# Performance work log

Measured on AMD Instinct MI355X. Metric: run time of the kernel, lower is better.

## Reference

```python
import jax, jax.numpy as jnp
import numpy as np

B, T, C, H = 4, 2048, 1024, 16
D = C // H


def setup_inputs() -> dict:
    key = jax.random.key(0)
    ks = jax.random.split(key, 5)
    s = C ** -0.5  # keep linear outputs O(1) like standard init
    x = jax.random.normal(ks[0], (B, T, C), dtype=jnp.float32)
    Wq = jax.random.normal(ks[1], (C, C), dtype=jnp.float32) * s
    Wk = jax.random.normal(ks[2], (C, C), dtype=jnp.float32) * s
    Wv = jax.random.normal(ks[3], (C, C), dtype=jnp.float32) * s
    Wproj = jax.random.normal(ks[4], (C, C), dtype=jnp.float32) * s
    alpha_raw = jnp.zeros((1, H, 1, 1), dtype=jnp.float32)
    beta_raw = jnp.zeros((1, H, 1, 1), dtype=jnp.float32)
    state = jnp.zeros((B, H, D, D), dtype=jnp.float32)
    return dict(x=x, Wq=Wq, Wk=Wk, Wv=Wv, Wproj=Wproj,
                alpha_raw=alpha_raw, beta_raw=beta_raw, state=state)


def reference(x, Wq, Wk, Wv, Wproj, alpha_raw, beta_raw, state):
    Bx, Tx, Cx = x.shape
    Hn = alpha_raw.shape[1]
    Dh = Cx // Hn
    # projections (torch Linear: x @ W^T), split heads -> (B, H, T, D)
    def proj(W):
        return (x @ W.T).reshape(Bx, Tx, Hn, Dh).transpose(0, 2, 1, 3)
    q, k, v = proj(Wq), proj(Wk), proj(Wv)
    # F.normalize(k, dim=-1) with eps=1e-12
    k = k / jnp.maximum(jnp.linalg.norm(k, axis=-1, keepdims=True), 1e-12)
    alpha = jax.nn.sigmoid(alpha_raw) * 0.5  # (1, H, 1, 1)
    beta = jax.nn.sigmoid(beta_raw) * 0.5

    def step(st, qkv):
        qt, kt, vt = qkv  # each (B, H, D)
        # y_t = q_t @ state^T
        y = jnp.einsum('bhe,bhde->bhd', qt, st)
        # Mk = state @ k_t
        Mk = jnp.einsum('bhde,bhe->bhd', st, kt)
        st = st - alpha * jnp.einsum('bhd,bhe->bhde', Mk, kt) \
                + beta * jnp.einsum('bhd,bhe->bhde', vt, kt)
        return st, y

    # scan over time: (T, B, H, D)
    qT = q.transpose(2, 0, 1, 3)
    kT = k.transpose(2, 0, 1, 3)
    vT = v.transpose(2, 0, 1, 3)
    state_f, ys = jax.lax.scan(step, state, (qT, kT, vT))
    y = ys.transpose(1, 0, 2, 3).reshape(Bx, Tx, Cx)  # (B, T, C)
    out = y @ Wproj.T
    return out, state_f
```

## Files before the change

kernel.cpp:

```cpp
#include <hip/hip_runtime.h>
#include <hip/hip_bf16.h>
#include <cstdint>

#define B_ 4
#define T_ 2048
#define C_ 1024
#define H_ 16
#define D_ 64
#define NC_ 32
#define L_ 64

typedef __attribute__((ext_vector_type(8))) short bf16x8;
typedef __attribute__((ext_vector_type(4))) float f32x4;

static __device__ __forceinline__ unsigned short f2bf(float f) {
  unsigned u = __float_as_uint(f);
  u += 0x7fff + ((u >> 16) & 1);
  return (unsigned short)(u >> 16);
}
static __device__ __forceinline__ float bf2f(unsigned short b) {
  return __uint_as_float(((unsigned)b) << 16);
}
static __device__ __forceinline__ int swz128(int row, int byte) {
  return row * 128 + (byte ^ ((row & 7) << 4));
}

__global__ __launch_bounds__(256) void cvt_kernel(const float* __restrict__ src,
                                                  unsigned short* __restrict__ dst, int n) {
  int i = (blockIdx.x * 256 + threadIdx.x) * 4;
  if (i >= n) return;
  float4 v = *reinterpret_cast<const float4*>(src + i);
  ushort4 o;
  o.x = f2bf(v.x); o.y = f2bf(v.y); o.z = f2bf(v.z); o.w = f2bf(v.w);
  *reinterpret_cast<ushort4*>(dst + i) = o;
}

template<int OUT_BF16>
__global__ __launch_bounds__(256) void gemm_bt(const unsigned short* __restrict__ A,
                                               const unsigned short* __restrict__ Bw,
                                               void* __restrict__ Cp,
                                               int M, int N, int K) {
  __shared__ __align__(16) unsigned short sA[128 * 32];
  __shared__ __align__(16) unsigned short sB[128 * 32];
  const int tid = threadIdx.x;
  const int wid = tid >> 6, lane = tid & 63;
  const int wm = wid >> 1, wn = wid & 1;
  const long blockM = (long)blockIdx.y * 128;
  const long blockN = (long)blockIdx.x * 128;

  f32x4 acc[4][4] = {};

  const int ar = lane >> 2;
  const int ac = (lane & 3) * 8;
  const unsigned short* Abase = A + (blockM + wid * 32 + ar) * (long)K + ac;
  const unsigned short* Bbase = Bw + (blockN + wid * 32 + ar) * (long)K + ac;
  char* sAb = (char*)sA + wid * 2048;
  char* sBb = (char*)sB + wid * 2048;

  for (int k0 = 0; k0 < K; k0 += 32) {
    __syncthreads();
    __builtin_amdgcn_global_load_lds((const __attribute__((address_space(1))) void*)(Abase + k0),
                                     (__attribute__((address_space(3))) void*)(sAb), 16, 0, 0);
    __builtin_amdgcn_global_load_lds((const __attribute__((address_space(1))) void*)(Abase + 16 * (long)K + k0),
                                     (__attribute__((address_space(3))) void*)(sAb + 1024), 16, 0, 0);
    __builtin_amdgcn_global_load_lds((const __attribute__((address_space(1))) void*)(Bbase + k0),
                                     (__attribute__((address_space(3))) void*)(sBb), 16, 0, 0);
    __builtin_amdgcn_global_load_lds((const __attribute__((address_space(1))) void*)(Bbase + 16 * (long)K + k0),
                                     (__attribute__((address_space(3))) void*)(sBb + 1024), 16, 0, 0);
    __syncthreads();

    const int koff = (lane >> 4) * 8;
    const int rA = wm * 64 + (lane & 15);
    const int rB = wn * 64 + (lane & 15);
    bf16x8 af[4], bfr[4];
#pragma unroll
    for (int m = 0; m < 4; ++m)
      af[m] = *reinterpret_cast<const bf16x8*>(&sA[(rA + m * 16) * 32 + koff]);
#pragma unroll
    for (int n = 0; n < 4; ++n)
      bfr[n] = *reinterpret_cast<const bf16x8*>(&sB[(rB + n * 16) * 32 + koff]);
#pragma unroll
    for (int m = 0; m < 4; ++m)
#pragma unroll
      for (int n = 0; n < 4; ++n)
        acc[m][n] = __builtin_amdgcn_mfma_f32_16x16x32_bf16(af[m], bfr[n], acc[m][n], 0, 0, 0);
  }

  const int cr = (lane >> 4) * 4;
  const int cc = lane & 15;
#pragma unroll
  for (int m = 0; m < 4; ++m) {
    long R = blockM + wm * 64 + m * 16 + cr;
#pragma unroll
    for (int n = 0; n < 4; ++n) {
      long Cc = blockN + wn * 64 + n * 16 + cc;
#pragma unroll
      for (int r = 0; r < 4; ++r) {
        if (OUT_BF16)
          ((unsigned short*)Cp)[(R + r) * (long)N + Cc] = f2bf(acc[m][n][r]);
        else
          ((float*)Cp)[(R + r) * (long)N + Cc] = acc[m][n][r];
      }
    }
  }
}

__global__ __launch_bounds__(256) void chunk_prep(
    unsigned short* __restrict__ qkv,
    const float* __restrict__ a_raw, const float* __restrict__ b_raw,
    unsigned short* __restrict__ Ubuf, unsigned short* __restrict__ Wbuf,
    unsigned short* __restrict__ SLbuf) {
  __shared__ __align__(16) unsigned short sK[64 * 64];
  __shared__ __align__(16) unsigned short sQ[64 * 64];
  __shared__ __align__(16) unsigned short sV[64 * 64];
  __shared__ float sA[64 * 64];

  const int blk = blockIdx.x;
  const int bh = blk >> 5, c = blk & 31;
  const int b = bh >> 4, h = bh & 15;
  const int tid = threadIdx.x;
  const int wid = tid >> 6, lane = tid & 63;

  const float alpha = 0.5f / (1.f + __expf(-a_raw[h]));
  const float beta  = 0.5f / (1.f + __expf(-b_raw[h]));

  {
    const int row = tid >> 2, cg = tid & 3;
    unsigned short* gp = qkv + (long)(b * 2048 + c * 64 + row) * 3072 + h * 64 + cg * 16;
    bf16x8 q0 = *(const bf16x8*)(gp);
    bf16x8 q1 = *(const bf16x8*)(gp + 8);
    bf16x8 k0 = *(const bf16x8*)(gp + 1024);
    bf16x8 k1 = *(const bf16x8*)(gp + 1024 + 8);
    bf16x8 v0 = *(const bf16x8*)(gp + 2048);
    bf16x8 v1 = *(const bf16x8*)(gp + 2048 + 8);
    float kf[16];
    float ss = 0.f;
#pragma unroll
    for (int i = 0; i < 8; ++i) { kf[i] = bf2f((unsigned short)k0[i]); ss += kf[i] * kf[i]; }
#pragma unroll
    for (int i = 0; i < 8; ++i) { kf[8 + i] = bf2f((unsigned short)k1[i]); ss += kf[8 + i] * kf[8 + i]; }
    ss += __shfl_xor(ss, 1);
    ss += __shfl_xor(ss, 2);
    const float inv = 1.f / fmaxf(sqrtf(ss), 1e-12f);
    bf16x8 n0, n1;
#pragma unroll
    for (int i = 0; i < 8; ++i) { n0[i] = (short)f2bf(kf[i] * inv); n1[i] = (short)f2bf(kf[8 + i] * inv); }
    *(bf16x8*)((char*)sK + swz128(row, cg * 32)) = n0;
    *(bf16x8*)((char*)sK + swz128(row, cg * 32 + 16)) = n1;
    *(bf16x8*)(gp + 1024) = n0;
    *(bf16x8*)(gp + 1024 + 8) = n1;
    *(bf16x8*)((char*)sQ + swz128(row, cg * 32)) = q0;
    *(bf16x8*)((char*)sQ + swz128(row, cg * 32 + 16)) = q1;
    *(bf16x8*)((char*)sV + row * 128 + cg * 32) = v0;
    *(bf16x8*)((char*)sV + row * 128 + cg * 32 + 16) = v1;
  }
  __syncthreads();

  const int rfrag = lane & 15, koff = (lane >> 4) * 8, crow = (lane >> 4) * 4;
  const int w2 = wid & 1;
  if (wid < 2) {
#pragma unroll
    for (int mt = 0; mt < 2; ++mt) {
      const int m = w2 * 2 + mt;
      const int ra = 16 * m + rfrag;
      f32x4 acc[4] = {};
#pragma unroll
      for (int ks = 0; ks < 2; ++ks) {
        bf16x8 af = *(const bf16x8*)((const char*)sK + swz128(ra, ks * 64 + koff * 2));
#pragma unroll
        for (int n = 0; n < 4; ++n) {
          bf16x8 bf = *(const bf16x8*)((const char*)sK + swz128(16 * n + rfrag, ks * 64 + koff * 2));
          acc[n] = __builtin_amdgcn_mfma_f32_16x16x32_bf16(af, bf, acc[n], 0, 0, 0);
        }
      }
#pragma unroll
      for (int n = 0; n < 4; ++n)
#pragma unroll
        for (int r = 0; r < 4; ++r)
          sA[(16 * m + crow + r) * 64 + 16 * n + rfrag] = acc[n][r];
    }
  } else {
#pragma unroll
    for (int mt = 0; mt < 2; ++mt) {
      const int m = w2 * 2 + mt;
      const int ra = 16 * m + rfrag;
      f32x4 acc[4] = {};
#pragma unroll
      for (int ks = 0; ks < 2; ++ks) {
        bf16x8 af = *(const bf16x8*)((const char*)sQ + swz128(ra, ks * 64 + koff * 2));
#pragma unroll
        for (int n = 0; n < 4; ++n) {
          bf16x8 bf = *(const bf16x8*)((const char*)sK + swz128(16 * n + rfrag, ks * 64 + koff * 2));
          acc[n] = __builtin_amdgcn_mfma_f32_16x16x32_bf16(af, bf, acc[n], 0, 0, 0);
        }
      }
#pragma unroll
      for (int n = 0; n < 4; ++n)
#pragma unroll
        for (int r = 0; r < 4; ++r) {
          int t = 16 * m + crow + r, j = 16 * n + rfrag;
          SLbuf[(long)blk * 4096 + t * 64 + j] = (j < t) ? f2bf(acc[n][r]) : (unsigned short)0;
        }
    }
  }
  __syncthreads();

  if (wid < 2) {
    const int d = lane;
    float x[64];
#pragma unroll
    for (int t = 0; t < 64; ++t) {
      float rhs;
      if (wid == 0) rhs = beta * bf2f(sV[t * 64 + d]);
      else          rhs = alpha * bf2f(*(const unsigned short*)((const char*)sK + swz128(t, 2 * d)));
      float s = 0.f;
#pragma unroll
      for (int j = 0; j < t; ++j) s = fmaf(sA[t * 64 + j], x[j], s);
      x[t] = rhs - alpha * s;
    }
    unsigned short* ob = (wid == 0 ? Ubuf : Wbuf) + (long)blk * 4096 + d;
#pragma unroll
    for (int t = 0; t < 64; ++t) ob[t * 64] = f2bf(x[t]);
  }
}

__global__ __launch_bounds__(256) void chunk_scan(
    const unsigned short* __restrict__ qkv,
    const unsigned short* __restrict__ Ubuf, const unsigned short* __restrict__ Wbuf,
    const unsigned short* __restrict__ SLbuf,
    const float* __restrict__ state_in, unsigned short* __restrict__ ybuf,
    float* __restrict__ state_out) {
  __shared__ __align__(16) unsigned short sQ[64 * 64];
  __shared__ __align__(16) unsigned short sW[64 * 64];
  __shared__ __align__(16) unsigned short sSL[64 * 64];
  __shared__ __align__(16) unsigned short sKT[64 * 64];
  __shared__ __align__(16) unsigned short sU[64 * 32];
  __shared__ __align__(16) unsigned short sGT[32 * 64];
  __shared__ __align__(16) unsigned short sS[32 * 64];

  const int blk = blockIdx.x;
  const int bh = blk >> 1, dh = blk & 1;
  const int b = bh >> 4, h = bh & 15;
  const int tid = threadIdx.x, wid = tid >> 6, lane = tid & 63;
  const int rfrag = lane & 15, koff = (lane >> 4) * 8, crow = (lane >> 4) * 4;
  const int row = tid >> 2, cg = tid & 3;

  const unsigned short* gpb = qkv + (long)(b * 2048 + row) * 3072 + h * 64 + cg * 16;
  const long tbb = ((long)(bh * 32) * 64 + row) * 64 + cg * 16;
  const long ubb = ((long)(bh * 32) * 64 + row) * 64 + dh * 32 + cg * 8;

  bf16x8 qv0, qv1, kv0, kv1, wv0, wv1, sl0, sl1, uv;
  {
    const unsigned short* gp = gpb;
    qv0 = *(const bf16x8*)gp;
    qv1 = *(const bf16x8*)(gp + 8);
    kv0 = *(const bf16x8*)(gp + 1024);
    kv1 = *(const bf16x8*)(gp + 1024 + 8);
    wv0 = *(const bf16x8*)(Wbuf + tbb);
    wv1 = *(const bf16x8*)(Wbuf + tbb + 8);
    sl0 = *(const bf16x8*)(SLbuf + tbb);
    sl1 = *(const bf16x8*)(SLbuf + tbb + 8);
    uv  = *(const bf16x8*)(Ubuf + ubb);
  }

  const int mS = wid & 1, nS0 = (wid >> 1) * 2;
  f32x4 sacc[2];
#pragma unroll
  for (int nn = 0; nn < 2; ++nn)
#pragma unroll
    for (int r = 0; r < 4; ++r)
      sacc[nn][r] = state_in[(long)bh * 4096 + (dh * 32 + 16 * mS + crow + r) * 64 + 16 * (nS0 + nn) + rfrag];
#pragma unroll
  for (int nn = 0; nn < 2; ++nn)
#pragma unroll
    for (int r = 0; r < 4; ++r) {
      int dr = 16 * mS + crow + r, e = 16 * (nS0 + nn) + rfrag;
      *(unsigned short*)((char*)sS + swz128(dr, 2 * e)) = f2bf(sacc[nn][r]);
    }

  for (int c = 0; c < NC_; ++c) {
    *(bf16x8*)((char*)sQ + swz128(row, cg * 32)) = qv0;
    *(bf16x8*)((char*)sQ + swz128(row, cg * 32 + 16)) = qv1;
    *(bf16x8*)((char*)sW + swz128(row, cg * 32)) = wv0;
    *(bf16x8*)((char*)sW + swz128(row, cg * 32 + 16)) = wv1;
    *(bf16x8*)((char*)sSL + swz128(row, cg * 32)) = sl0;
    *(bf16x8*)((char*)sSL + swz128(row, cg * 32 + 16)) = sl1;
#pragma unroll
    for (int i = 0; i < 8; ++i) {
      *(unsigned short*)((char*)sKT + swz128(cg * 16 + i, 2 * row)) = (unsigned short)kv0[i];
      *(unsigned short*)((char*)sKT + swz128(cg * 16 + 8 + i, 2 * row)) = (unsigned short)kv1[i];
    }
    *(bf16x8*)((char*)sU + (row * 32 + cg * 8) * 2) = uv;

    {
      const int cn = (c + 1 < NC_) ? c + 1 : c;
      const unsigned short* gp = gpb + (long)cn * 64 * 3072;
      const long tb = tbb + (long)cn * 4096;
      qv0 = *(const bf16x8*)gp;
      qv1 = *(const bf16x8*)(gp + 8);
      kv0 = *(const bf16x8*)(gp + 1024);
      kv1 = *(const bf16x8*)(gp + 1024 + 8);
      wv0 = *(const bf16x8*)(Wbuf + tb);
      wv1 = *(const bf16x8*)(Wbuf + tb + 8);
      sl0 = *(const bf16x8*)(SLbuf + tb);
      sl1 = *(const bf16x8*)(SLbuf + tb + 8);
      uv  = *(const bf16x8*)(Ubuf + ubb + (long)cn * 4096);
    }
    __syncthreads();

    const int ta = 16 * wid + rfrag;
    f32x4 p[2] = {};
    f32x4 yac[2] = {};
#pragma unroll
    for (int ks = 0; ks < 2; ++ks) {
      bf16x8 afw = *(const bf16x8*)((const char*)sW + swz128(ta, ks * 64 + koff * 2));
      bf16x8 afq = *(const bf16x8*)((const char*)sQ + swz128(ta, ks * 64 + koff * 2));
#pragma unroll
      for (int n = 0; n < 2; ++n) {
        bf16x8 bf = *(const bf16x8*)((const char*)sS + swz128(16 * n + rfrag, ks * 64 + koff * 2));
        p[n] = __builtin_amdgcn_mfma_f32_16x16x32_bf16(afw, bf, p[n], 0, 0, 0);
        yac[n] = __builtin_amdgcn_mfma_f32_16x16x32_bf16(afq, bf, yac[n], 0, 0, 0);
      }
    }
#pragma unroll
    for (int n = 0; n < 2; ++n)
#pragma unroll
      for (int r = 0; r < 4; ++r) {
        int t = 16 * wid + crow + r, dl = 16 * n + rfrag;
        float g = bf2f(sU[t * 32 + dl]) - p[n][r];
        *(unsigned short*)((char*)sGT + swz128(dl, 2 * t)) = f2bf(g);
      }
    __syncthreads();

#pragma unroll
    for (int ks = 0; ks < 2; ++ks) {
      bf16x8 af = *(const bf16x8*)((const char*)sSL + swz128(ta, ks * 64 + koff * 2));
#pragma unroll
      for (int n = 0; n < 2; ++n) {
        bf16x8 bf = *(const bf16x8*)((const char*)sGT + swz128(16 * n + rfrag, ks * 64 + koff * 2));
        yac[n] = __builtin_amdgcn_mfma_f32_16x16x32_bf16(af, bf, yac[n], 0, 0, 0);
      }
    }
#pragma unroll
    for (int n = 0; n < 2; ++n)
#pragma unroll
      for (int r = 0; r < 4; ++r) {
        int t = 16 * wid + crow + r;
        ybuf[(long)(b * 2048 + c * 64 + t) * 1024 + h * 64 + dh * 32 + 16 * n + rfrag] = f2bf(yac[n][r]);
      }
#pragma unroll
    for (int ks = 0; ks < 2; ++ks) {
      bf16x8 af = *(const bf16x8*)((const char*)sGT + swz128(16 * mS + rfrag, ks * 64 + koff * 2));
#pragma unroll
      for (int nn = 0; nn < 2; ++nn) {
        bf16x8 bf = *(const bf16x8*)((const char*)sKT + swz128(16 * (nS0 + nn) + rfrag, ks * 64 + koff * 2));
        sacc[nn] = __builtin_amdgcn_mfma_f32_16x16x32_bf16(af, bf, sacc[nn], 0, 0, 0);
      }
    }
    __syncthreads();
#pragma unroll
    for (int nn = 0; nn < 2; ++nn)
#pragma unroll
      for (int r = 0; r < 4; ++r) {
        int dr = 16 * mS + crow + r, e = 16 * (nS0 + nn) + rfrag;
        *(unsigned short*)((char*)sS + swz128(dr, 2 * e)) = f2bf(sacc[nn][r]);
      }
  }

#pragma unroll
  for (int nn = 0; nn < 2; ++nn)
#pragma unroll
    for (int r = 0; r < 4; ++r)
      state_out[(long)bh * 4096 + (dh * 32 + 16 * mS + crow + r) * 64 + 16 * (nS0 + nn) + rfrag] = sacc[nn][r];
}

extern "C" void kernel_launch(void* const* d_in, const int* in_sizes, int n_in,
                              void* d_out, int out_size, void* d_ws, size_t ws_size,
                              hipStream_t stream) {
  (void)in_sizes; (void)n_in; (void)out_size; (void)ws_size;
  const float* x     = (const float*)d_in[0];
  const float* Wq    = (const float*)d_in[1];
  const float* Wk    = (const float*)d_in[2];
  const float* Wv    = (const float*)d_in[3];
  const float* Wproj = (const float*)d_in[4];
  const float* a_raw = (const float*)d_in[5];
  const float* b_raw = (const float*)d_in[6];
  const float* state = (const float*)d_in[7];

  char* ws = (char*)d_ws;
  unsigned short* xbf = (unsigned short*)ws;
  unsigned short* W3  = (unsigned short*)(ws + (16l << 20));
  unsigned short* Wp  = (unsigned short*)(ws + (22l << 20));
  unsigned short* qkv = (unsigned short*)(ws + (24l << 20));
  unsigned short* Ub  = (unsigned short*)(ws + (72l << 20));
  unsigned short* Wb  = (unsigned short*)(ws + (88l << 20));
  unsigned short* SLb = (unsigned short*)(ws + (104l << 20));
  float* out = (float*)d_out;
  float* state_out = out + (long)B_ * T_ * C_;

  cvt_kernel<<<dim3(8192), dim3(256), 0, stream>>>(x, xbf, 8388608);
  cvt_kernel<<<dim3(1024), dim3(256), 0, stream>>>(Wq, W3, 1048576);
  cvt_kernel<<<dim3(1024), dim3(256), 0, stream>>>(Wk, W3 + 1048576, 1048576);
  cvt_kernel<<<dim3(1024), dim3(256), 0, stream>>>(Wv, W3 + 2097152, 1048576);
  cvt_kernel<<<dim3(1024), dim3(256), 0, stream>>>(Wproj, Wp, 1048576);

  gemm_bt<1><<<dim3(3072 / 128, 8192 / 128), dim3(256), 0, stream>>>(xbf, W3, (void*)qkv, 8192, 3072, 1024);

  chunk_prep<<<dim3(2048), dim3(256), 0, stream>>>(qkv, a_raw, b_raw, Ub, Wb, SLb);
  chunk_scan<<<dim3(128), dim3(256), 0, stream>>>(qkv, Ub, Wb, SLb, state, xbf, state_out);

  gemm_bt<0><<<dim3(1024 / 128, 8192 / 128), dim3(256), 0, stream>>>(xbf, Wp, (void*)out, 8192, 1024, 1024);
}
```

Measured before the change: 216.2 us.

## Split chunk scan state rows four ways and merge weight conversions

The sequential chunk_scan kernel now splits each head's 64-row state into four 16-row slices instead of two 32-row halves. This doubles the grid from 128 to 256 blocks, so more of the GPU's compute units take part in the serial scan and each block does less MFMA work per chunk. The cost is redundant work: every block still loads and stages the full Q, K, W and SL tiles, so global and LDS traffic per head roughly doubles. Separately, the four weight-conversion launches are merged into one kernel to cut launch overhead.

```diff
diff --git a/kernel.cpp b/kernel.cpp
--- a/kernel.cpp
+++ b/kernel.cpp
@@ -29,6 +29,22 @@
                                                   unsigned short* __restrict__ dst, int n) {
   int i = (blockIdx.x * 256 + threadIdx.x) * 4;
   if (i >= n) return;
+  float4 v = *reinterpret_cast<const float4*>(src + i);
+  ushort4 o;
+  o.x = f2bf(v.x); o.y = f2bf(v.y); o.z = f2bf(v.z); o.w = f2bf(v.w);
+  *reinterpret_cast<ushort4*>(dst + i) = o;
+}
+
+__global__ __launch_bounds__(256) void cvt_w_kernel(const float* __restrict__ wq,
+                                                    const float* __restrict__ wk,
+                                                    const float* __restrict__ wv,
+                                                    const float* __restrict__ wp,
+                                                    unsigned short* __restrict__ W3,
+                                                    unsigned short* __restrict__ Wp) {
+  const int g = blockIdx.x >> 10;
+  const float* src = (g == 0) ? wq : (g == 1) ? wk : (g == 2) ? wv : wp;
+  unsigned short* dst = (g < 3) ? (W3 + (long)g * 1048576) : Wp;
+  int i = ((blockIdx.x & 1023) * 256 + threadIdx.x) * 4;
   float4 v = *reinterpret_cast<const float4*>(src + i);
   ushort4 o;
   o.x = f2bf(v.x); o.y = f2bf(v.y); o.z = f2bf(v.z); o.w = f2bf(v.w);
@@ -234,12 +250,12 @@
   __shared__ __align__(16) unsigned short sW[64 * 64];
   __shared__ __align__(16) unsigned short sSL[64 * 64];
   __shared__ __align__(16) unsigned short sKT[64 * 64];
-  __shared__ __align__(16) unsigned short sU[64 * 32];
-  __shared__ __align__(16) unsigned short sGT[32 * 64];
-  __shared__ __align__(16) unsigned short sS[32 * 64];
+  __shared__ __align__(16) unsigned short sU[64 * 16];
+  __shared__ __align__(16) unsigned short sGT[16 * 64];
+  __shared__ __align__(16) unsigned short sS[16 * 64];
 
   const int blk = blockIdx.x;
-  const int bh = blk >> 1, dh = blk & 1;
+  const int bh = blk >> 2, dq = blk & 3;
   const int b = bh >> 4, h = bh & 15;
   const int tid = threadIdx.x, wid = tid >> 6, lane = tid & 63;
   const int rfrag = lane & 15, koff = (lane >> 4) * 8, crow = (lane >> 4) * 4;
@@ -247,36 +263,28 @@
 
   const unsigned short* gpb = qkv + (long)(b * 2048 + row) * 3072 + h * 64 + cg * 16;
   const long tbb = ((long)(bh * 32) * 64 + row) * 64 + cg * 16;
-  const long ubb = ((long)(bh * 32) * 64 + row) * 64 + dh * 32 + cg * 8;
+  const long ubb = ((long)(bh * 32) * 64 + (tid >> 1)) * 64 + dq * 16 + (tid & 1) * 8;
 
   bf16x8 qv0, qv1, kv0, kv1, wv0, wv1, sl0, sl1, uv;
   {
-    const unsigned short* gp = gpb;
-    qv0 = *(const bf16x8*)gp;
-    qv1 = *(const bf16x8*)(gp + 8);
-    kv0 = *(const bf16x8*)(gp + 1024);
-    kv1 = *(const bf16x8*)(gp + 1024 + 8);
+    qv0 = *(const bf16x8*)gpb;
+    qv1 = *(const bf16x8*)(gpb + 8);
+    kv0 = *(const bf16x8*)(gpb + 1024);
+    kv1 = *(const bf16x8*)(gpb + 1024 + 8);
     wv0 = *(const bf16x8*)(Wbuf + tbb);
     wv1 = *(const bf16x8*)(Wbuf + tbb + 8);
     sl0 = *(const bf16x8*)(SLbuf + tbb);
     sl1 = *(const bf16x8*)(SLbuf + tbb + 8);
-    uv  = *(const bf16x8*)(Ubuf + ubb);
-  }
-
-  const int mS = wid & 1, nS0 = (wid >> 1) * 2;
-  f32x4 sacc[2];
-#pragma unroll
-  for (int nn = 0; nn < 2; ++nn)
-#pragma unroll
-    for (int r = 0; r < 4; ++r)
-      sacc[nn][r] = state_in[(long)bh * 4096 + (dh * 32 + 16 * mS + crow + r) * 64 + 16 * (nS0 + nn) + rfrag];
-#pragma unroll
-  for (int nn = 0; nn < 2; ++nn)
-#pragma unroll
-    for (int r = 0; r < 4; ++r) {
-      int dr = 16 * mS + crow + r, e = 16 * (nS0 + nn) + rfrag;
-      *(unsigned short*)((char*)sS + swz128(dr, 2 * e)) = f2bf(sacc[nn][r]);
-    }
+    uv = (tid < 128) ? *(const bf16x8*)(Ubuf + ubb) : bf16x8{};
+  }
+
+  f32x4 sacc;
+#pragma unroll
+  for (int r = 0; r < 4; ++r)
+    sacc[r] = state_in[(long)bh * 4096 + (dq * 16 + crow + r) * 64 + 16 * wid + rfrag];
+#pragma unroll
+  for (int r = 0; r < 4; ++r)
+    *(unsigned short*)((char*)sS + swz128(crow + r, 2 * (16 * wid + rfrag))) = f2bf(sacc[r]);
 
   for (int c = 0; c < NC_; ++c) {
     *(bf16x8*)((char*)sQ + swz128(row, cg * 32)) = qv0;
@@ -290,7 +298,7 @@
       *(unsigned short*)((char*)sKT + swz128(cg * 16 + i, 2 * row)) = (unsigned short)kv0[i];
       *(unsigned short*)((char*)sKT + swz128(cg * 16 + 8 + i, 2 * row)) = (unsigned short)kv1[i];
     }
-    *(bf16x8*)((char*)sU + (row * 32 + cg * 8) * 2) = uv;
+    if (tid < 128) *(bf16x8*)((char*)sU + ((tid >> 1) * 16 + (tid & 1) * 8) * 2) = uv;
 
     {
       const int cn = (c + 1 < NC_) ? c + 1 : c;
@@ -304,74 +312,55 @@
       wv1 = *(const bf16x8*)(Wbuf + tb + 8);
       sl0 = *(const bf16x8*)(SLbuf + tb);
       sl1 = *(const bf16x8*)(SLbuf + tb + 8);
-      uv  = *(const bf16x8*)(Ubuf + ubb + (long)cn * 4096);
+      if (tid < 128) uv = *(const bf16x8*)(Ubuf + ubb + (long)cn * 4096);
     }
     __syncthreads();
 
     const int ta = 16 * wid + rfrag;
-    f32x4 p[2] = {};
-    f32x4 yac[2] = {};
+    f32x4 p = {};
+    f32x4 yac = {};
 #pragma unroll
     for (int ks = 0; ks < 2; ++ks) {
       bf16x8 afw = *(const bf16x8*)((const char*)sW + swz128(ta, ks * 64 + koff * 2));
       bf16x8 afq = *(const bf16x8*)((const char*)sQ + swz128(ta, ks * 64 + koff * 2));
-#pragma unroll
-      for (int n = 0; n < 2; ++n) {
-        bf16x8 bf = *(const bf16x8*)((const char*)sS + swz128(16 * n + rfrag, ks * 64 + koff * 2));
-        p[n] = __builtin_amdgcn_mfma_f32_16x16x32_bf16(afw, bf, p[n], 0, 0, 0);
-        yac[n] = __builtin_amdgcn_mfma_f32_16x16x32_bf16(afq, bf, yac[n], 0, 0, 0);
-      }
-    }
-#pragma unroll
-    for (int n = 0; n < 2; ++n)
-#pragma unroll
-      for (int r = 0; r < 4; ++r) {
-        int t = 16 * wid + crow + r, dl = 16 * n + rfrag;
-        float g = bf2f(sU[t * 32 + dl]) - p[n][r];
-        *(unsigned short*)((char*)sGT + swz128(dl, 2 * t)) = f2bf(g);
-      }
+      bf16x8 bS = *(const bf16x8*)((const char*)sS + swz128(rfrag, ks * 64 + koff * 2));
+      p = __builtin_amdgcn_mfma_f32_16x16x32_bf16(afw, bS, p, 0, 0, 0);
+      yac = __builtin_amdgcn_mfma_f32_16x16x32_bf16(afq, bS, yac, 0, 0, 0);
+    }
+#pragma unroll
+    for (int r = 0; r < 4; ++r) {
+      int t = 16 * wid + crow + r;
+      float g = bf2f(sU[t * 16 + rfrag]) - p[r];
+      *(unsigned short*)((char*)sGT + swz128(rfrag, 2 * t)) = f2bf(g);
+    }
     __syncthreads();
 
 #pragma unroll
     for (int ks = 0; ks < 2; ++ks) {
-      bf16x8 af = *(const bf16x8*)((const char*)sSL + swz128(ta, ks * 64 + koff * 2));
-#pragma unroll
-      for (int n = 0; n < 2; ++n) {
-        bf16x8 bf = *(const bf16x8*)((const char*)sGT + swz128(16 * n + rfrag, ks * 64 + koff * 2));
-        yac[n] = __builtin_amdgcn_mfma_f32_16x16x32_bf16(af, bf, yac[n], 0, 0, 0);
-      }
-    }
-#pragma unroll
-    for (int n = 0; n < 2; ++n)
-#pragma unroll
-      for (int r = 0; r < 4; ++r) {
-        int t = 16 * wid + crow + r;
-        ybuf[(long)(b * 2048 + c * 64 + t) * 1024 + h * 64 + dh * 32 + 16 * n + rfrag] = f2bf(yac[n][r]);
-      }
+      bf16x8 aSL = *(const bf16x8*)((const char*)sSL + swz128(ta, ks * 64 + koff * 2));
+      bf16x8 bGT = *(const bf16x8*)((const char*)sGT + swz128(rfrag, ks * 64 + koff * 2));
+      yac = __builtin_amdgcn_mfma_f32_16x16x32_bf16(aSL, bGT, yac, 0, 0, 0);
+    }
+#pragma unroll
+    for (int r = 0; r < 4; ++r) {
+      int t = 16 * wid + crow + r;
+      ybuf[(long)(b * 2048 + c * 64 + t) * 1024 + h * 64 + dq * 16 + rfrag] = f2bf(yac[r]);
+    }
 #pragma unroll
     for (int ks = 0; ks < 2; ++ks) {
-      bf16x8 af = *(const bf16x8*)((const char*)sGT + swz128(16 * mS + rfrag, ks * 64 + koff * 2));
-#pragma unroll
-      for (int nn = 0; nn < 2; ++nn) {
-        bf16x8 bf = *(const bf16x8*)((const char*)sKT + swz128(16 * (nS0 + nn) + rfrag, ks * 64 + koff * 2));
-        sacc[nn] = __builtin_amdgcn_mfma_f32_16x16x32_bf16(af, bf, sacc[nn], 0, 0, 0);
-      }
-    }
-    __syncthreads();
-#pragma unroll
-    for (int nn = 0; nn < 2; ++nn)
-#pragma unroll
-      for (int r = 0; r < 4; ++r) {
-        int dr = 16 * mS + crow + r, e = 16 * (nS0 + nn) + rfrag;
-        *(unsigned short*)((char*)sS + swz128(dr, 2 * e)) = f2bf(sacc[nn][r]);
-      }
-  }
-
-#pragma unroll
-  for (int nn = 0; nn < 2; ++nn)
+      bf16x8 aGT = *(const bf16x8*)((const char*)sGT + swz128(rfrag, ks * 64 + koff * 2));
+      bf16x8 bKT = *(const bf16x8*)((const char*)sKT + swz128(16 * wid + rfrag, ks * 64 + koff * 2));
+      sacc = __builtin_amdgcn_mfma_f32_16x16x32_bf16(aGT, bKT, sacc, 0, 0, 0);
+    }
+    __syncthreads();
 #pragma unroll
     for (int r = 0; r < 4; ++r)
-      state_out[(long)bh * 4096 + (dh * 32 + 16 * mS + crow + r) * 64 + 16 * (nS0 + nn) + rfrag] = sacc[nn][r];
+      *(unsigned short*)((char*)sS + swz128(crow + r, 2 * (16 * wid + rfrag))) = f2bf(sacc[r]);
+  }
+
+#pragma unroll
+  for (int r = 0; r < 4; ++r)
+    state_out[(long)bh * 4096 + (dq * 16 + crow + r) * 64 + 16 * wid + rfrag] = sacc[r];
 }
 
 extern "C" void kernel_launch(void* const* d_in, const int* in_sizes, int n_in,
@@ -399,15 +388,12 @@
   float* state_out = out + (long)B_ * T_ * C_;
 
   cvt_kernel<<<dim3(8192), dim3(256), 0, stream>>>(x, xbf, 8388608);
-  cvt_kernel<<<dim3(1024), dim3(256), 0, stream>>>(Wq, W3, 1048576);
-  cvt_kernel<<<dim3(1024), dim3(256), 0, stream>>>(Wk, W3 + 1048576, 1048576);
-  cvt_kernel<<<dim3(1024), dim3(256), 0, stream>>>(Wv, W3 + 2097152, 1048576);
-  cvt_kernel<<<dim3(1024), dim3(256), 0, stream>>>(Wproj, Wp, 1048576);
+  cvt_w_kernel<<<dim3(4096), dim3(256), 0, stream>>>(Wq, Wk, Wv, Wproj, W3, Wp);
 
   gemm_bt<1><<<dim3(3072 / 128, 8192 / 128), dim3(256), 0, stream>>>(xbf, W3, (void*)qkv, 8192, 3072, 1024);
 
   chunk_prep<<<dim3(2048), dim3(256), 0, stream>>>(qkv, a_raw, b_raw, Ub, Wb, SLb);
-  chunk_scan<<<dim3(128), dim3(256), 0, stream>>>(qkv, Ub, Wb, SLb, state, xbf, state_out);
+  chunk_scan<<<dim3(256), dim3(256), 0, stream>>>(qkv, Ub, Wb, SLb, state, xbf, state_out);
 
   gemm_bt<0><<<dim3(1024 / 128, 8192 / 128), dim3(256), 0, stream>>>(xbf, Wp, (void*)out, 8192, 1024, 1024);
 }
```

New measurement: 211.8 us. -2.0%, faster.
